# Optimization experiments

Measured on AMD Instinct MI355X. Metric: run time of the kernel, lower is better.

## Reference

```python
import jax, jax.numpy as jnp
import numpy as np

HEADS = 16
HIDDEN = 1024
D_K = HIDDEN // HEADS


def setup_inputs() -> dict:
    key = jax.random.key(0)
    ks = jax.random.split(key, 13)
    B, S, H = 2, 2048, HIDDEN
    scale = 1.0 / np.sqrt(H)
    inp = {
        "q": jax.random.normal(ks[0], (B, S, H), jnp.float32),
        "k": jax.random.normal(ks[1], (B, S, H), jnp.float32),
        "v": jax.random.normal(ks[2], (B, S, H), jnp.float32),
        "mask": jax.random.randint(ks[3], (B, S, S), 0, 2, jnp.int32),
        # torch Linear weights: [out, in], y = x @ W.T + b
        "Wq": jax.random.normal(ks[4], (H, H), jnp.float32) * scale,
        "bq": jax.random.normal(ks[5], (H,), jnp.float32) * 0.01,
        "Wk": jax.random.normal(ks[6], (H, H), jnp.float32) * scale,
        "bk": jax.random.normal(ks[7], (H,), jnp.float32) * 0.01,
        "Wv": jax.random.normal(ks[8], (H, H), jnp.float32) * scale,
        "bv": jax.random.normal(ks[9], (H,), jnp.float32) * 0.01,
        "Wo": jax.random.normal(ks[10], (H, H), jnp.float32) * scale,
        "bo": jax.random.normal(ks[11], (H,), jnp.float32) * 0.01,
    }
    return inp


def _split_heads(x, B):
    # (B, S, H) -> (B, heads, S, d_k)
    return x.reshape(B, -1, HEADS, D_K).transpose(0, 2, 1, 3)


def reference(q, k, v, mask, Wq, bq, Wk, bk, Wv, bv, Wo, bo):
    B, S, H = q.shape
    qh = _split_heads(q @ Wq.T + bq, B)
    kh = _split_heads(k @ Wk.T + bk, B)
    vh = _split_heads(v @ Wv.T + bv, B)
    inv_sqrt_dk = 1.0 / jnp.sqrt(jnp.asarray(D_K, qh.dtype))
    logits = jnp.einsum("bhqd,bhkd->bhqk", qh, kh) * inv_sqrt_dk
    # faithful to source: masked positions get logit 1e-9 (not -inf)
    m = mask[:, None, :, :]  # broadcast over heads
    logits = jnp.where(m == 0, jnp.asarray(1e-9, logits.dtype), logits)
    scores = jax.nn.softmax(logits, axis=-1)
    o = jnp.einsum("bhqk,bhkd->bhqd", scores, vh)  # (B, heads, S, d_k)
    o = o.transpose(0, 2, 1, 3).reshape(B, S, H)
    return o @ Wo.T + bo
```

## Files before the change

### kernel.cpp

```cpp
#include <hip/hip_runtime.h>

#define SEQ   2048
#define NHEAD 16
#define DKK   64
#define HID   1024

typedef __attribute__((ext_vector_type(8))) short bf16x8;
typedef __attribute__((ext_vector_type(4))) float f32x4;

__device__ __forceinline__ unsigned short f32_bf16(float f) {
    unsigned int u = __builtin_bit_cast(unsigned int, f);
    u += 0x7fffu + ((u >> 16) & 1u);
    return (unsigned short)(u >> 16);
}

__device__ __forceinline__ unsigned int pack_bf16x2(float a, float b) {
    return (unsigned int)f32_bf16(a) | ((unsigned int)f32_bf16(b) << 16);
}

__device__ __forceinline__ float fast_exp2(float x) {
    float r;
    asm("v_exp_f32 %0, %1" : "=v"(r) : "v"(x));
    return r;
}

__device__ __forceinline__ void glds16(const void* g, void* l) {
    __builtin_amdgcn_global_load_lds(
        (const __attribute__((address_space(1))) unsigned int*)g,
        (__attribute__((address_space(3))) unsigned int*)l, 16, 0, 0);
}

__global__ __launch_bounds__(256)
void prep_kernel(const float* __restrict__ q, const float* __restrict__ k,
                 const float* __restrict__ v,
                 const float* __restrict__ Wq, const float* __restrict__ Wk,
                 const float* __restrict__ Wv, const float* __restrict__ Wo,
                 const int* __restrict__ mask,
                 unsigned short* __restrict__ ws, unsigned long long* __restrict__ Mb)
{
    const int bid = blockIdx.x;
    if (bid < 16384) {
        int i = bid * 256 + threadIdx.x;
        const float* src; int off;
        if (i < 1048576)      { src = q;  off = i; }
        else if (i < 2097152) { src = k;  off = i - 1048576; }
        else if (i < 3145728) { src = v;  off = i - 2097152; }
        else if (i < 3407872) { src = Wq; off = i - 3145728; }
        else if (i < 3670016) { src = Wk; off = i - 3407872; }
        else if (i < 3932160) { src = Wv; off = i - 3670016; }
        else                  { src = Wo; off = i - 3932160; }
        float4 a = ((const float4*)src)[off];
        ((uint2*)ws)[i] = make_uint2(pack_bf16x2(a.x, a.y), pack_bf16x2(a.z, a.w));
    } else {
        int idx = (bid - 16384) * 256 + threadIdx.x;
        const int* src = mask + (size_t)idx * 64;
        unsigned long long wv = 0;
        #pragma unroll
        for (int i = 0; i < 16; ++i) {
            int4 m4 = *(const int4*)(src + i * 4);
            wv |= (unsigned long long)(m4.x != 0) << (i * 4 + 0);
            wv |= (unsigned long long)(m4.y != 0) << (i * 4 + 1);
            wv |= (unsigned long long)(m4.z != 0) << (i * 4 + 2);
            wv |= (unsigned long long)(m4.w != 0) << (i * 4 + 3);
        }
        Mb[idx] = wv;
    }
}

__global__ __launch_bounds__(256, 2)
void proj_kernel(const unsigned short* __restrict__ xq, const unsigned short* __restrict__ xk,
                 const unsigned short* __restrict__ xv,
                 const unsigned short* __restrict__ Wqb, const unsigned short* __restrict__ Wkb,
                 const unsigned short* __restrict__ Wvb,
                 const float* __restrict__ bq_, const float* __restrict__ bk_,
                 const float* __restrict__ bv_,
                 unsigned short* __restrict__ Qh, unsigned short* __restrict__ Kh,
                 unsigned short* __restrict__ Vt)
{
    const int z = blockIdx.z;
    const unsigned short* X; const unsigned short* W; const float* bias;
    if (z == 0)      { X = xq; W = Wqb; bias = bq_; }
    else if (z == 1) { X = xk; W = Wkb; bias = bk_; }
    else             { X = xv; W = Wvb; bias = bv_; }

    const int m0 = blockIdx.x * 128;
    const int n0 = blockIdx.y * 128;
    const int tid  = threadIdx.x;
    const int lane = tid & 63, wid = tid >> 6;
    const int wm = (wid >> 1) * 64, wn = (wid & 1) * 64;
    const int l15 = lane & 15, quad = lane >> 4;

    __shared__ __align__(16) unsigned short As[128 * 32];
    __shared__ __align__(16) unsigned short Bs[128 * 32];

    const int r0 = tid >> 2, cg = tid & 3;
    const unsigned short* gA = X + (size_t)(m0 + r0) * HID + ((cg ^ (r0 & 3)) * 8);
    const unsigned short* gB = W + (size_t)(n0 + r0) * HID + ((cg ^ (r0 & 3)) * 8);
    unsigned short* lA0 = &As[tid * 8];
    unsigned short* lA1 = &As[(tid + 256) * 8];
    unsigned short* lB0 = &Bs[tid * 8];
    unsigned short* lB1 = &Bs[(tid + 256) * 8];

    const int cgsel = (quad ^ (l15 & 3)) * 8;

    f32x4 acc[4][4];
    #pragma unroll
    for (int i = 0; i < 4; ++i)
        #pragma unroll
        for (int j = 0; j < 4; ++j)
            acc[i][j] = f32x4{0.f, 0.f, 0.f, 0.f};

    for (int k0 = 0; k0 < HID; k0 += 32) {
        glds16(gA + k0, lA0);
        glds16(gA + (size_t)64 * HID + k0, lA1);
        glds16(gB + k0, lB0);
        glds16(gB + (size_t)64 * HID + k0, lB1);
        __syncthreads();

        bf16x8 af[4], bfr[4];
        #pragma unroll
        for (int mi = 0; mi < 4; ++mi)
            af[mi] = *(const bf16x8*)&As[(wm + mi * 16 + l15) * 32 + cgsel];
        #pragma unroll
        for (int ni = 0; ni < 4; ++ni)
            bfr[ni] = *(const bf16x8*)&Bs[(wn + ni * 16 + l15) * 32 + cgsel];
        #pragma unroll
        for (int mi = 0; mi < 4; ++mi)
            #pragma unroll
            for (int ni = 0; ni < 4; ++ni)
                acc[mi][ni] = __builtin_amdgcn_mfma_f32_16x16x32_bf16(
                    af[mi], bfr[ni], acc[mi][ni], 0, 0, 0);
        __syncthreads();
    }

    const float QSCALE = 0.18033688f;
    #pragma unroll
    for (int mi = 0; mi < 4; ++mi) {
        #pragma unroll
        for (int ni = 0; ni < 4; ++ni) {
            int n = n0 + wn + ni * 16 + l15;
            float bv = bias[n];
            int hh = n >> 6, d = n & 63;
            #pragma unroll
            for (int r = 0; r < 4; ++r) {
                int m = m0 + wm + mi * 16 + quad * 4 + r;
                int bb = m >> 11, s = m & 2047;
                float val = acc[mi][ni][r] + bv;
                if (z == 0)
                    Qh[((size_t)(bb * NHEAD + hh) * SEQ + s) * DKK + d] = f32_bf16(val * QSCALE);
                else if (z == 1)
                    Kh[((size_t)(bb * NHEAD + hh) * SEQ + s) * DKK + d] = f32_bf16(val);
                else
                    Vt[((size_t)(bb * NHEAD + hh) * DKK + d) * SEQ + s] = f32_bf16(val);
            }
        }
    }
}

__global__ __launch_bounds__(256, 4)
void attn_kernel(const unsigned short* __restrict__ Qh, const unsigned short* __restrict__ Kh,
                 const unsigned short* __restrict__ Vt,
                 const unsigned long long* __restrict__ Mb,
                 unsigned short* __restrict__ Om)
{
    const int qt = blockIdx.x;
    const int h  = blockIdx.y;
    const int b  = blockIdx.z;
    const int tid  = threadIdx.x;
    const int lane = tid & 63, w = tid >> 6;
    const int l15 = lane & 15, quad = lane >> 4;
    const int q0 = qt * 64;

    const size_t hoff = (size_t)(b * NHEAD + h) * SEQ * DKK;
    const unsigned short* Qp = Qh + hoff;
    const unsigned short* Kp = Kh + hoff;
    const unsigned short* Vp = Vt + hoff;

    __shared__ __align__(16) unsigned short Ks[2][64 * 64];
    __shared__ __align__(16) unsigned short Vs[2][64 * 64];
    __shared__ __align__(16) unsigned short Ps[4][16 * 64];

    const int sr0 = tid >> 3, ss0 = tid & 7;
    const int sr1 = sr0 + 32;
    const unsigned short* Kg0 = Kp + sr0 * DKK + ((ss0 ^ (sr0 & 7)) * 8);
    const unsigned short* Kg1 = Kp + sr1 * DKK + ((ss0 ^ (sr1 & 7)) * 8);
    const unsigned short* Vg0 = Vp + (size_t)sr0 * SEQ + ((ss0 ^ (sr0 & 7)) * 8);
    const unsigned short* Vg1 = Vp + (size_t)sr1 * SEQ + ((ss0 ^ (sr1 & 7)) * 8);

    const int swz0 = ((0 * 4 + quad) ^ (l15 & 7)) * 8;
    const int swz1 = ((1 * 4 + quad) ^ (l15 & 7)) * 8;

    const int xsw = l15 & 14;
    int wadr[4];
    #pragma unroll
    for (int ni = 0; ni < 4; ++ni)
        wadr[ni] = l15 * 64 + (((ni * 4 + quad) ^ xsw) * 4);
    const int padr0 = l15 * 64 + (((quad * 2) ^ xsw) * 4);
    const int padr1 = l15 * 64 + (((8 + quad * 2) ^ xsw) * 4);

    glds16(Kg0, &Ks[0][tid * 8]);
    glds16(Kg1, &Ks[0][2048 + tid * 8]);
    glds16(Vg0, &Vs[0][tid * 8]);
    glds16(Vg1, &Vs[0][2048 + tid * 8]);

    bf16x8 qf[2];
    #pragma unroll
    for (int kc = 0; kc < 2; ++kc)
        qf[kc] = *(const bf16x8*)(Qp + (size_t)(q0 + w * 16 + l15) * DKK + kc * 32 + quad * 8);

    bf16x8 onesf;
    #pragma unroll
    for (int i = 0; i < 8; ++i) onesf[i] = (short)0x3F80;

    f32x4 o_acc[4];
    f32x4 l_acc = f32x4{0.f, 0.f, 0.f, 0.f};
    #pragma unroll
    for (int nd = 0; nd < 4; ++nd) o_acc[nd] = f32x4{0.f, 0.f, 0.f, 0.f};

    const unsigned long long* Mrow =
        Mb + ((size_t)b * SEQ + q0 + w * 16 + l15) * (SEQ / 64);

    __syncthreads();

    for (int kt = 0; kt < SEQ / 64; ++kt) {
        const int cur = kt & 1;
        if (kt < SEQ / 64 - 1) {
            const int nb = cur ^ 1;
            glds16(Kg0 + (kt + 1) * 64 * DKK, &Ks[nb][tid * 8]);
            glds16(Kg1 + (kt + 1) * 64 * DKK, &Ks[nb][2048 + tid * 8]);
            glds16(Vg0 + (kt + 1) * 64,       &Vs[nb][tid * 8]);
            glds16(Vg1 + (kt + 1) * 64,       &Vs[nb][2048 + tid * 8]);
        }

        const unsigned long long mwq = Mrow[kt] >> (quad * 4);

        f32x4 st[4];
        #pragma unroll
        for (int ni = 0; ni < 4; ++ni) st[ni] = f32x4{0.f, 0.f, 0.f, 0.f};
        {
            bf16x8 kb[4];
            #pragma unroll
            for (int ni = 0; ni < 4; ++ni)
                kb[ni] = *(const bf16x8*)&Ks[cur][(ni * 16 + l15) * 64 + swz0];
            __builtin_amdgcn_s_setprio(1);
            #pragma unroll
            for (int ni = 0; ni < 4; ++ni)
                st[ni] = __builtin_amdgcn_mfma_f32_16x16x32_bf16(kb[ni], qf[0], st[ni], 0, 0, 0);
            __builtin_amdgcn_s_setprio(0);
            #pragma unroll
            for (int ni = 0; ni < 4; ++ni)
                kb[ni] = *(const bf16x8*)&Ks[cur][(ni * 16 + l15) * 64 + swz1];
            __builtin_amdgcn_s_setprio(1);
            #pragma unroll
            for (int ni = 0; ni < 4; ++ni)
                st[ni] = __builtin_amdgcn_mfma_f32_16x16x32_bf16(kb[ni], qf[1], st[ni], 0, 0, 0);
            __builtin_amdgcn_s_setprio(0);
        }

        #pragma unroll
        for (int ni = 0; ni < 4; ++ni) {
            const unsigned int b4 = (unsigned int)(mwq >> (ni * 16)) & 0xFu;
            float p0 = (b4 & 1u) ? fast_exp2(st[ni][0]) : 1.0f;
            float p1 = (b4 & 2u) ? fast_exp2(st[ni][1]) : 1.0f;
            float p2 = (b4 & 4u) ? fast_exp2(st[ni][2]) : 1.0f;
            float p3 = (b4 & 8u) ? fast_exp2(st[ni][3]) : 1.0f;
            *(uint2*)&Ps[w][wadr[ni]] = make_uint2(pack_bf16x2(p0, p1), pack_bf16x2(p2, p3));
        }

        {
            bf16x8 pa = *(const bf16x8*)&Ps[w][padr0];
            bf16x8 vb[4];
            #pragma unroll
            for (int nd = 0; nd < 4; ++nd)
                vb[nd] = *(const bf16x8*)&Vs[cur][(nd * 16 + l15) * 64 + swz0];
            __builtin_amdgcn_s_setprio(1);
            l_acc = __builtin_amdgcn_mfma_f32_16x16x32_bf16(pa, onesf, l_acc, 0, 0, 0);
            #pragma unroll
            for (int nd = 0; nd < 4; ++nd)
                o_acc[nd] = __builtin_amdgcn_mfma_f32_16x16x32_bf16(pa, vb[nd], o_acc[nd], 0, 0, 0);
            __builtin_amdgcn_s_setprio(0);

            pa = *(const bf16x8*)&Ps[w][padr1];
            #pragma unroll
            for (int nd = 0; nd < 4; ++nd)
                vb[nd] = *(const bf16x8*)&Vs[cur][(nd * 16 + l15) * 64 + swz1];
            __builtin_amdgcn_s_setprio(1);
            l_acc = __builtin_amdgcn_mfma_f32_16x16x32_bf16(pa, onesf, l_acc, 0, 0, 0);
            #pragma unroll
            for (int nd = 0; nd < 4; ++nd)
                o_acc[nd] = __builtin_amdgcn_mfma_f32_16x16x32_bf16(pa, vb[nd], o_acc[nd], 0, 0, 0);
            __builtin_amdgcn_s_setprio(0);
        }

        __syncthreads();
    }

    #pragma unroll
    for (int r = 0; r < 4; ++r) {
        float rinv = 1.0f / l_acc[r];
        int row = q0 + w * 16 + quad * 4 + r;
        #pragma unroll
        for (int nd = 0; nd < 4; ++nd)
            Om[((size_t)b * SEQ + row) * HID + h * DKK + nd * 16 + l15] =
                f32_bf16(o_acc[nd][r] * rinv);
    }
}

__global__ __launch_bounds__(256, 2)
void outproj_kernel(const unsigned short* __restrict__ Om, const unsigned short* __restrict__ Wob,
                    const float* __restrict__ bo_, float* __restrict__ out)
{
    const int m0 = blockIdx.x * 128;
    const int n0 = blockIdx.y * 128;
    const int tid  = threadIdx.x;
    const int lane = tid & 63, wid = tid >> 6;
    const int wm = (wid >> 1) * 64, wn = (wid & 1) * 64;
    const int l15 = lane & 15, quad = lane >> 4;

    __shared__ __align__(16) unsigned short As[128 * 32];
    __shared__ __align__(16) unsigned short Bs[128 * 32];

    const int r0 = tid >> 2, cg = tid & 3;
    const unsigned short* gA = Om + (size_t)(m0 + r0) * HID + ((cg ^ (r0 & 3)) * 8);
    const unsigned short* gB = Wob + (size_t)(n0 + r0) * HID + ((cg ^ (r0 & 3)) * 8);
    unsigned short* lA0 = &As[tid * 8];
    unsigned short* lA1 = &As[(tid + 256) * 8];
    unsigned short* lB0 = &Bs[tid * 8];
    unsigned short* lB1 = &Bs[(tid + 256) * 8];
    const int cgsel = (quad ^ (l15 & 3)) * 8;

    f32x4 acc[4][4];
    #pragma unroll
    for (int i = 0; i < 4; ++i)
        #pragma unroll
        for (int j = 0; j < 4; ++j)
            acc[i][j] = f32x4{0.f, 0.f, 0.f, 0.f};

    for (int k0 = 0; k0 < HID; k0 += 32) {
        glds16(gA + k0, lA0);
        glds16(gA + (size_t)64 * HID + k0, lA1);
        glds16(gB + k0, lB0);
        glds16(gB + (size_t)64 * HID + k0, lB1);
        __syncthreads();

        bf16x8 af[4], bfr[4];
        #pragma unroll
        for (int mi = 0; mi < 4; ++mi)
            af[mi] = *(const bf16x8*)&As[(wm + mi * 16 + l15) * 32 + cgsel];
        #pragma unroll
        for (int ni = 0; ni < 4; ++ni)
            bfr[ni] = *(const bf16x8*)&Bs[(wn + ni * 16 + l15) * 32 + cgsel];
        #pragma unroll
        for (int mi = 0; mi < 4; ++mi)
            #pragma unroll
            for (int ni = 0; ni < 4; ++ni)
                acc[mi][ni] = __builtin_amdgcn_mfma_f32_16x16x32_bf16(
                    af[mi], bfr[ni], acc[mi][ni], 0, 0, 0);
        __syncthreads();
    }

    #pragma unroll
    for (int mi = 0; mi < 4; ++mi) {
        #pragma unroll
        for (int ni = 0; ni < 4; ++ni) {
            int n = n0 + wn + ni * 16 + l15;
            float bv = bo_[n];
            #pragma unroll
            for (int r = 0; r < 4; ++r) {
                int m = m0 + wm + mi * 16 + quad * 4 + r;
                out[(size_t)m * HID + n] = acc[mi][ni][r] + bv;
            }
        }
    }
}

extern "C" void kernel_launch(void* const* d_in, const int* in_sizes, int n_in,
                              void* d_out, int out_size, void* d_ws, size_t ws_size,
                              hipStream_t stream) {
    const float* q    = (const float*)d_in[0];
    const float* k    = (const float*)d_in[1];
    const float* v    = (const float*)d_in[2];
    const int*   mask = (const int*)  d_in[3];
    const float* Wq   = (const float*)d_in[4];
    const float* bq   = (const float*)d_in[5];
    const float* Wk   = (const float*)d_in[6];
    const float* bk   = (const float*)d_in[7];
    const float* Wv   = (const float*)d_in[8];
    const float* bv   = (const float*)d_in[9];
    const float* Wo   = (const float*)d_in[10];
    const float* bo   = (const float*)d_in[11];
    float* out = (float*)d_out;

    unsigned short* ws  = (unsigned short*)d_ws;
    unsigned short* qb  = ws;
    unsigned short* kbx = ws + 4194304;
    unsigned short* vbx = ws + 8388608;
    unsigned short* Wqb = ws + 12582912;
    unsigned short* Wkb = ws + 13631488;
    unsigned short* Wvb = ws + 14680064;
    unsigned short* Wob = ws + 15728640;
    unsigned short* Qh  = ws + 16777216;
    unsigned short* Kh  = ws + 20971520;
    unsigned short* Vt  = ws + 25165824;
    unsigned short* Om  = ws;
    unsigned long long* Mb = (unsigned long long*)(ws + 29360128);

    prep_kernel<<<dim3(16896), 256, 0, stream>>>(q, k, v, Wq, Wk, Wv, Wo, mask, ws, Mb);

    proj_kernel<<<dim3(32, 8, 3), 256, 0, stream>>>(qb, kbx, vbx, Wqb, Wkb, Wvb,
                                                    bq, bk, bv, Qh, Kh, Vt);
    attn_kernel<<<dim3(32, NHEAD, 2), 256, 0, stream>>>(Qh, Kh, Vt, Mb, Om);
    outproj_kernel<<<dim3(32, 8, 1), 256, 0, stream>>>(Om, Wob, bo, out);
}
```

Baseline: 292.2 us.

## Double-buffer GEMM loads, add V transpose kernel, retile out-projection, packed bf16 convert

The projection and output-projection GEMMs now double-buffer their LDS tiles, so the next K-slice is fetched while the current one runs on MFMA, and they raise wave priority around the MFMA block. The V projection stores V in head-major layout into the output buffer as scratch, and a new transpose kernel writes Vt, replacing the strided scattered stores in the GEMM epilogue. The output projection uses 128x64 tiles to launch twice as many blocks. The software bf16 rounding is replaced with the hardware v_cvt_pk_bf16_f32 instruction. The cost is an extra kernel launch, extra V traffic, and double the LDS footprint.

```diff
diff --git a/kernel.cpp b/kernel.cpp
--- a/kernel.cpp
+++ b/kernel.cpp
@@ -14,8 +14,10 @@
     return (unsigned short)(u >> 16);
 }
 
-__device__ __forceinline__ unsigned int pack_bf16x2(float a, float b) {
-    return (unsigned int)f32_bf16(a) | ((unsigned int)f32_bf16(b) << 16);
+__device__ __forceinline__ unsigned int cvt_pk_bf16(float lo, float hi) {
+    unsigned int r;
+    asm("v_cvt_pk_bf16_f32 %0, %1, %2" : "=v"(r) : "v"(lo), "v"(hi));
+    return r;
 }
 
 __device__ __forceinline__ float fast_exp2(float x) {
@@ -50,7 +52,7 @@
         else if (i < 3932160) { src = Wv; off = i - 3670016; }
         else                  { src = Wo; off = i - 3932160; }
         float4 a = ((const float4*)src)[off];
-        ((uint2*)ws)[i] = make_uint2(pack_bf16x2(a.x, a.y), pack_bf16x2(a.z, a.w));
+        ((uint2*)ws)[i] = make_uint2(cvt_pk_bf16(a.x, a.y), cvt_pk_bf16(a.z, a.w));
     } else {
         int idx = (bid - 16384) * 256 + threadIdx.x;
         const int* src = mask + (size_t)idx * 64;
@@ -75,7 +77,7 @@
                  const float* __restrict__ bq_, const float* __restrict__ bk_,
                  const float* __restrict__ bv_,
                  unsigned short* __restrict__ Qh, unsigned short* __restrict__ Kh,
-                 unsigned short* __restrict__ Vt)
+                 unsigned short* __restrict__ Vh)
 {
     const int z = blockIdx.z;
     const unsigned short* X; const unsigned short* W; const float* bias;
@@ -90,16 +92,12 @@
     const int wm = (wid >> 1) * 64, wn = (wid & 1) * 64;
     const int l15 = lane & 15, quad = lane >> 4;
 
-    __shared__ __align__(16) unsigned short As[128 * 32];
-    __shared__ __align__(16) unsigned short Bs[128 * 32];
+    __shared__ __align__(16) unsigned short As[2][128 * 32];
+    __shared__ __align__(16) unsigned short Bs[2][128 * 32];
 
     const int r0 = tid >> 2, cg = tid & 3;
     const unsigned short* gA = X + (size_t)(m0 + r0) * HID + ((cg ^ (r0 & 3)) * 8);
     const unsigned short* gB = W + (size_t)(n0 + r0) * HID + ((cg ^ (r0 & 3)) * 8);
-    unsigned short* lA0 = &As[tid * 8];
-    unsigned short* lA1 = &As[(tid + 256) * 8];
-    unsigned short* lB0 = &Bs[tid * 8];
-    unsigned short* lB1 = &Bs[(tid + 256) * 8];
 
     const int cgsel = (quad ^ (l15 & 3)) * 8;
 
@@ -110,26 +108,37 @@
         for (int j = 0; j < 4; ++j)
             acc[i][j] = f32x4{0.f, 0.f, 0.f, 0.f};
 
+    glds16(gA, &As[0][tid * 8]);
+    glds16(gA + (size_t)64 * HID, &As[0][(tid + 256) * 8]);
+    glds16(gB, &Bs[0][tid * 8]);
+    glds16(gB + (size_t)64 * HID, &Bs[0][(tid + 256) * 8]);
+    __syncthreads();
+
     for (int k0 = 0; k0 < HID; k0 += 32) {
-        glds16(gA + k0, lA0);
-        glds16(gA + (size_t)64 * HID + k0, lA1);
-        glds16(gB + k0, lB0);
-        glds16(gB + (size_t)64 * HID + k0, lB1);
-        __syncthreads();
+        const int cur = (k0 >> 5) & 1;
+        if (k0 + 32 < HID) {
+            const int nb = cur ^ 1;
+            glds16(gA + k0 + 32, &As[nb][tid * 8]);
+            glds16(gA + (size_t)64 * HID + k0 + 32, &As[nb][(tid + 256) * 8]);
+            glds16(gB + k0 + 32, &Bs[nb][tid * 8]);
+            glds16(gB + (size_t)64 * HID + k0 + 32, &Bs[nb][(tid + 256) * 8]);
+        }
 
         bf16x8 af[4], bfr[4];
         #pragma unroll
         for (int mi = 0; mi < 4; ++mi)
-            af[mi] = *(const bf16x8*)&As[(wm + mi * 16 + l15) * 32 + cgsel];
+            af[mi] = *(const bf16x8*)&As[cur][(wm + mi * 16 + l15) * 32 + cgsel];
         #pragma unroll
         for (int ni = 0; ni < 4; ++ni)
-            bfr[ni] = *(const bf16x8*)&Bs[(wn + ni * 16 + l15) * 32 + cgsel];
+            bfr[ni] = *(const bf16x8*)&Bs[cur][(wn + ni * 16 + l15) * 32 + cgsel];
+        __builtin_amdgcn_s_setprio(1);
         #pragma unroll
         for (int mi = 0; mi < 4; ++mi)
             #pragma unroll
             for (int ni = 0; ni < 4; ++ni)
                 acc[mi][ni] = __builtin_amdgcn_mfma_f32_16x16x32_bf16(
                     af[mi], bfr[ni], acc[mi][ni], 0, 0, 0);
+        __builtin_amdgcn_s_setprio(0);
         __syncthreads();
     }
 
@@ -151,9 +160,55 @@
                 else if (z == 1)
                     Kh[((size_t)(bb * NHEAD + hh) * SEQ + s) * DKK + d] = f32_bf16(val);
                 else
-                    Vt[((size_t)(bb * NHEAD + hh) * DKK + d) * SEQ + s] = f32_bf16(val);
+                    Vh[((size_t)(bb * NHEAD + hh) * SEQ + s) * DKK + d] = f32_bf16(val);
             }
         }
+    }
+}
+
+__global__ __launch_bounds__(256)
+void vtrans_kernel(const unsigned short* __restrict__ Vh, unsigned short* __restrict__ Vt)
+{
+    __shared__ unsigned int T[64 * 32];
+    const int bh = blockIdx.y;
+    const int s0 = blockIdx.x * 64;
+    const int tid = threadIdx.x;
+    const unsigned short* src = Vh + ((size_t)bh * SEQ + s0) * DKK;
+    unsigned short* dst = Vt + (size_t)bh * DKK * SEQ + s0;
+
+    #pragma unroll
+    for (int j = 0; j < 2; ++j) {
+        int i = tid + j * 256;
+        int s = i >> 3, ch = i & 7;
+        uint4 d4 = *(const uint4*)(src + (size_t)s * DKK + ch * 8);
+        *(uint4*)&T[s * 32 + 4 * (ch ^ (s >> 3))] = d4;
+    }
+    __syncthreads();
+    #pragma unroll
+    for (int j = 0; j < 2; ++j) {
+        int i = tid + j * 256;
+        int d = i >> 3, sb = (i & 7) * 8;
+        int d2 = d >> 1, hi = d & 1;
+        int g = d2 >> 2, w4 = d2 & 3;
+        unsigned int r[8];
+        #pragma unroll
+        for (int kk = 0; kk < 8; ++kk) {
+            int s = sb + kk;
+            r[kk] = T[s * 32 + 4 * (g ^ (s >> 3)) + w4];
+        }
+        uint4 ov;
+        if (hi) {
+            ov.x = (r[0] >> 16) | (r[1] & 0xffff0000u);
+            ov.y = (r[2] >> 16) | (r[3] & 0xffff0000u);
+            ov.z = (r[4] >> 16) | (r[5] & 0xffff0000u);
+            ov.w = (r[6] >> 16) | (r[7] & 0xffff0000u);
+        } else {
+            ov.x = (r[0] & 0xffffu) | (r[1] << 16);
+            ov.y = (r[2] & 0xffffu) | (r[3] << 16);
+            ov.z = (r[4] & 0xffffu) | (r[5] << 16);
+            ov.w = (r[6] & 0xffffu) | (r[7] << 16);
+        }
+        *(uint4*)(dst + (size_t)d * SEQ + sb) = ov;
     }
 }
 
@@ -264,7 +319,7 @@
             float p1 = (b4 & 2u) ? fast_exp2(st[ni][1]) : 1.0f;
             float p2 = (b4 & 4u) ? fast_exp2(st[ni][2]) : 1.0f;
             float p3 = (b4 & 8u) ? fast_exp2(st[ni][3]) : 1.0f;
-            *(uint2*)&Ps[w][wadr[ni]] = make_uint2(pack_bf16x2(p0, p1), pack_bf16x2(p2, p3));
+            *(uint2*)&Ps[w][wadr[ni]] = make_uint2(cvt_pk_bf16(p0, p1), cvt_pk_bf16(p2, p3));
         }
 
         {
@@ -311,58 +366,63 @@
                     const float* __restrict__ bo_, float* __restrict__ out)
 {
     const int m0 = blockIdx.x * 128;
-    const int n0 = blockIdx.y * 128;
+    const int n0 = blockIdx.y * 64;
     const int tid  = threadIdx.x;
     const int lane = tid & 63, wid = tid >> 6;
-    const int wm = (wid >> 1) * 64, wn = (wid & 1) * 64;
+    const int wm = (wid >> 1) * 64, wn = (wid & 1) * 32;
     const int l15 = lane & 15, quad = lane >> 4;
 
-    __shared__ __align__(16) unsigned short As[128 * 32];
-    __shared__ __align__(16) unsigned short Bs[128 * 32];
+    __shared__ __align__(16) unsigned short As[2][128 * 32];
+    __shared__ __align__(16) unsigned short Bs[2][64 * 32];
 
     const int r0 = tid >> 2, cg = tid & 3;
     const unsigned short* gA = Om + (size_t)(m0 + r0) * HID + ((cg ^ (r0 & 3)) * 8);
     const unsigned short* gB = Wob + (size_t)(n0 + r0) * HID + ((cg ^ (r0 & 3)) * 8);
-    unsigned short* lA0 = &As[tid * 8];
-    unsigned short* lA1 = &As[(tid + 256) * 8];
-    unsigned short* lB0 = &Bs[tid * 8];
-    unsigned short* lB1 = &Bs[(tid + 256) * 8];
     const int cgsel = (quad ^ (l15 & 3)) * 8;
 
-    f32x4 acc[4][4];
+    f32x4 acc[4][2];
     #pragma unroll
     for (int i = 0; i < 4; ++i)
         #pragma unroll
-        for (int j = 0; j < 4; ++j)
+        for (int j = 0; j < 2; ++j)
             acc[i][j] = f32x4{0.f, 0.f, 0.f, 0.f};
 
+    glds16(gA, &As[0][tid * 8]);
+    glds16(gA + (size_t)64 * HID, &As[0][(tid + 256) * 8]);
+    glds16(gB, &Bs[0][tid * 8]);
+    __syncthreads();
+
     for (int k0 = 0; k0 < HID; k0 += 32) {
-        glds16(gA + k0, lA0);
-        glds16(gA + (size_t)64 * HID + k0, lA1);
-        glds16(gB + k0, lB0);
-        glds16(gB + (size_t)64 * HID + k0, lB1);
-        __syncthreads();
-
-        bf16x8 af[4], bfr[4];
+        const int cur = (k0 >> 5) & 1;
+        if (k0 + 32 < HID) {
+            const int nb = cur ^ 1;
+            glds16(gA + k0 + 32, &As[nb][tid * 8]);
+            glds16(gA + (size_t)64 * HID + k0 + 32, &As[nb][(tid + 256) * 8]);
+            glds16(gB + k0 + 32, &Bs[nb][tid * 8]);
+        }
+
+        bf16x8 af[4], bfr[2];
         #pragma unroll
         for (int mi = 0; mi < 4; ++mi)
-            af[mi] = *(const bf16x8*)&As[(wm + mi * 16 + l15) * 32 + cgsel];
-        #pragma unroll
-        for (int ni = 0; ni < 4; ++ni)
-            bfr[ni] = *(const bf16x8*)&Bs[(wn + ni * 16 + l15) * 32 + cgsel];
+            af[mi] = *(const bf16x8*)&As[cur][(wm + mi * 16 + l15) * 32 + cgsel];
+        #pragma unroll
+        for (int ni = 0; ni < 2; ++ni)
+            bfr[ni] = *(const bf16x8*)&Bs[cur][(wn + ni * 16 + l15) * 32 + cgsel];
+        __builtin_amdgcn_s_setprio(1);
         #pragma unroll
         for (int mi = 0; mi < 4; ++mi)
             #pragma unroll
-            for (int ni = 0; ni < 4; ++ni)
+            for (int ni = 0; ni < 2; ++ni)
                 acc[mi][ni] = __builtin_amdgcn_mfma_f32_16x16x32_bf16(
                     af[mi], bfr[ni], acc[mi][ni], 0, 0, 0);
+        __builtin_amdgcn_s_setprio(0);
         __syncthreads();
     }
 
     #pragma unroll
     for (int mi = 0; mi < 4; ++mi) {
         #pragma unroll
-        for (int ni = 0; ni < 4; ++ni) {
+        for (int ni = 0; ni < 2; ++ni) {
             int n = n0 + wn + ni * 16 + l15;
             float bv = bo_[n];
             #pragma unroll
@@ -404,11 +464,13 @@
     unsigned short* Vt  = ws + 25165824;
     unsigned short* Om  = ws;
     unsigned long long* Mb = (unsigned long long*)(ws + 29360128);
+    unsigned short* Vh  = (unsigned short*)d_out;
 
     prep_kernel<<<dim3(16896), 256, 0, stream>>>(q, k, v, Wq, Wk, Wv, Wo, mask, ws, Mb);
 
     proj_kernel<<<dim3(32, 8, 3), 256, 0, stream>>>(qb, kbx, vbx, Wqb, Wkb, Wvb,
-                                                    bq, bk, bv, Qh, Kh, Vt);
+                                                    bq, bk, bv, Qh, Kh, Vh);
+    vtrans_kernel<<<dim3(32, 32), 256, 0, stream>>>(Vh, Vt);
     attn_kernel<<<dim3(32, NHEAD, 2), 256, 0, stream>>>(Qh, Kh, Vt, Mb, Om);
-    outproj_kernel<<<dim3(32, 8, 1), 256, 0, stream>>>(Om, Wob, bo, out);
-}
+    outproj_kernel<<<dim3(32, 16), 256, 0, stream>>>(Om, Wob, bo, out);
+}
```

After: 279.3 us. -4.4%, faster.
